# Performance work log

Hardware: AMD Instinct MI355X
Metric: run time of the kernel (lower is better)

Reference implementation:

```python
import jax, jax.numpy as jnp
import numpy as np

N_HEAD = 16

def setup_inputs() -> dict:
    key = jax.random.key(0)
    k1, k2, k3 = jax.random.split(key, 3)
    B, S, D = 2, 2048, 1024
    x = jax.random.normal(k1, (B, S, D), dtype=jnp.float32)
    w_attn = jax.random.normal(k2, (D, 3 * D), dtype=jnp.float32) * 0.02
    b_attn = jnp.zeros((3 * D,), dtype=jnp.float32)
    w_proj = jax.random.normal(k3, (D, D), dtype=jnp.float32) * 0.02
    b_proj = jnp.zeros((D,), dtype=jnp.float32)
    return {"x": x, "w_attn": w_attn, "b_attn": b_attn, "w_proj": w_proj, "b_proj": b_proj}

def reference(x, w_attn, b_attn, w_proj, b_proj):
    B, S, D = x.shape
    hd = D // N_HEAD
    qkv = x @ w_attn + b_attn                      # [B,S,3D]
    q, k, v = jnp.split(qkv, 3, axis=-1)
    def heads(t):  # [B,S,D] -> [B,H,S,hd]
        return t.reshape(B, S, N_HEAD, hd).transpose(0, 2, 1, 3)
    q, k, v = heads(q), heads(k), heads(v)
    # NOTE: original forward applies NO scaling and NO causal mask; dropout=eval (identity)
    scores = jnp.einsum('bhqd,bhkd->bhqk', q, k)   # [B,H,S,S]
    probs = jax.nn.softmax(scores, axis=-1)
    out = jnp.einsum('bhqk,bhkd->bhqd', probs, v)  # [B,H,S,hd]
    out = out.transpose(0, 2, 1, 3).reshape(B, S, D)
    return out @ w_proj + b_proj
```

## Files before the change

### kernel.cpp

```cpp
#include <hip/hip_runtime.h>

typedef _Float16 f16;
typedef _Float16 f16x8 __attribute__((ext_vector_type(8)));
typedef _Float16 f16x4 __attribute__((ext_vector_type(4)));
typedef float    f32x4 __attribute__((ext_vector_type(4)));
typedef unsigned int u32;
typedef unsigned int u32x4 __attribute__((ext_vector_type(4)));

#define LOG2E 1.44269504088896340736f
#define EXPC  (13.0f * 1.44269504088896340736f)

__device__ __forceinline__ void gload_lds16(const void* g, void* l) {
  __builtin_amdgcn_global_load_lds(
      (const __attribute__((address_space(1))) void*)g,
      (__attribute__((address_space(3))) void*)l, 16, 0, 0);
}

__device__ __forceinline__ void block_sync() {
  asm volatile("" ::: "memory");
  __builtin_amdgcn_s_barrier();
  asm volatile("" ::: "memory");
}

__global__ void k_cast_x(const float* __restrict__ in, f16* __restrict__ out) {
  int i = blockIdx.x * blockDim.x + threadIdx.x;
  f32x4 v = ((const f32x4*)in)[i];
  f16x4 o;
  o[0] = (f16)v[0]; o[1] = (f16)v[1]; o[2] = (f16)v[2]; o[3] = (f16)v[3];
  ((f16x4*)out)[i] = o;
}

__global__ void k_transpose_cast(const float* __restrict__ in, f16* __restrict__ out,
                                 int R, int C) {
  __shared__ float tile[32][33];
  int c0 = blockIdx.x * 32, r0 = blockIdx.y * 32;
  int tx = threadIdx.x, ty = threadIdx.y;
#pragma unroll
  for (int i = 0; i < 4; i++)
    tile[ty + i * 8][tx] = in[(size_t)(r0 + ty + i * 8) * C + c0 + tx];
  __syncthreads();
#pragma unroll
  for (int i = 0; i < 4; i++)
    out[(size_t)(c0 + ty + i * 8) * R + r0 + tx] = (f16)tile[tx][ty + i * 8];
}

template <int EPI>
__global__ __launch_bounds__(256)
void k_gemm(const f16* __restrict__ A, const f16* __restrict__ BT,
            const float* __restrict__ bias,
            f16* __restrict__ out_qk, f16* __restrict__ out_vT,
            float* __restrict__ out_f) {
  constexpr int K = 1024;
  __shared__ f16 smem[4][128 * 64];
  const int t = threadIdx.x;
  const int l = t & 63;
  const int w = t >> 6;
  const int wm = (w >> 1) * 64;
  const int wn = (w & 1) * 64;
  const int m0 = blockIdx.x * 128;
  const int n0 = blockIdx.y * 128;
  const int lr = l & 15;
  const int lk = (l >> 4) * 8;

  const f16* Ap = A + (size_t)(m0 + (t >> 3)) * K + ((t & 7) << 3);
  const f16* Bp = BT + (size_t)(n0 + (t >> 3)) * K + ((t & 7) << 3);

#define GSTAGE(buf) do { \
    _Pragma("unroll") \
    for (int i2 = 0; i2 < 4; i2++) \
      gload_lds16(Ap + (size_t)(i2 * 32) * K, &smem[buf][(i2 * 256 + t) * 8]); \
    _Pragma("unroll") \
    for (int i2 = 0; i2 < 4; i2++) \
      gload_lds16(Bp + (size_t)(i2 * 32) * K, &smem[2 + buf][(i2 * 256 + t) * 8]); \
    Ap += 64; Bp += 64; } while (0)

  f32x4 acc[4][4] = {};

#define GCOMPUTE(buf) do { \
    _Pragma("unroll") \
    for (int kk = 0; kk < 64; kk += 32) { \
      f16x8 af[4], bf[4]; \
      _Pragma("unroll") \
      for (int i = 0; i < 4; i++) \
        af[i] = *(const f16x8*)&smem[buf][(wm + i * 16 + lr) * 64 + kk + lk]; \
      _Pragma("unroll") \
      for (int j = 0; j < 4; j++) \
        bf[j] = *(const f16x8*)&smem[2 + buf][(wn + j * 16 + lr) * 64 + kk + lk]; \
      _Pragma("unroll") \
      for (int i = 0; i < 4; i++) \
        _Pragma("unroll") \
        for (int j = 0; j < 4; j++) \
          acc[i][j] = __builtin_amdgcn_mfma_f32_16x16x32_f16(af[i], bf[j], acc[i][j], 0, 0, 0); \
    } } while (0)

  GSTAGE(0);
  asm volatile("s_waitcnt vmcnt(0)" ::: "memory");
  block_sync();

  for (int kt = 0; kt < 16; kt += 2) {
    GSTAGE(1);
    GCOMPUTE(0);
    asm volatile("s_waitcnt vmcnt(0)" ::: "memory");
    block_sync();
    if (kt + 2 < 16) GSTAGE(0);
    GCOMPUTE(1);
    asm volatile("s_waitcnt vmcnt(0)" ::: "memory");
    block_sync();
  }
#undef GSTAGE
#undef GCOMPUTE

  if (EPI == 1) {
#pragma unroll
    for (int i = 0; i < 4; i++) {
      int mbase = m0 + wm + i * 16 + (l >> 4) * 4;
#pragma unroll
      for (int j = 0; j < 4; j++) {
        int n = n0 + wn + j * 16 + lr;
        float bv = bias[n];
#pragma unroll
        for (int r = 0; r < 4; r++)
          out_f[(size_t)(mbase + r) * 1024 + n] = acc[i][j][r] + bv;
      }
    }
  } else if (n0 < 2048) {
#pragma unroll
    for (int i = 0; i < 4; i++) {
      int mbase = m0 + wm + i * 16 + (l >> 4) * 4;
#pragma unroll
      for (int j = 0; j < 4; j++) {
        int n = n0 + wn + j * 16 + lr;
        float bv = bias[n];
        float sc = (n0 + wn + j * 16 < 1024) ? LOG2E : 1.0f;
#pragma unroll
        for (int r = 0; r < 4; r++)
          out_qk[(size_t)(mbase + r) * 2048 + n] = (f16)((acc[i][j][r] + bv) * sc);
      }
    }
  } else {
    f16* scr = &smem[0][0];
#pragma unroll
    for (int i = 0; i < 4; i++) {
      int s0 = wm + i * 16 + (l >> 4) * 4;
#pragma unroll
      for (int j = 0; j < 4; j++) {
        int nl = wn + j * 16 + lr;
        float bv = bias[n0 + nl];
        f16x4 pv;
#pragma unroll
        for (int r = 0; r < 4; r++) pv[r] = (f16)(acc[i][j][r] + bv);
        *(f16x4*)&scr[nl * 128 + (s0 ^ ((nl & 15) << 3))] = pv;
      }
    }
    block_sync();
    const int b = m0 >> 11;
    const int sbase = m0 & 2047;
#pragma unroll
    for (int p = 0; p < 8; p++) {
      int nl = (t >> 4) + p * 16;
      int sc = (t & 15) << 3;
      f16x8 vv = *(const f16x8*)&scr[nl * 128 + (sc ^ ((nl & 15) << 3))];
      int ng = (n0 - 2048) + nl;
      int hg = ng >> 6, d = ng & 63;
      *(f16x8*)&out_vT[(((size_t)(b * 16 + hg) * 64 + d) << 11) + sbase + sc] = vv;
    }
  }
}

__global__ __launch_bounds__(256, 2)
void k_attn(const f16* __restrict__ qk, const f16* __restrict__ vT,
            f16* __restrict__ aout) {
  __shared__ f16 Kl[2][64 * 64];
  __shared__ f16 Vl[2][64 * 64];
  const int t = threadIdx.x;
  const int l = t & 63;
  const int w = t >> 6;
  const int lr = l & 15;
  const int lg = l >> 4;
  const int lk = lg * 8;

  const int o  = (blockIdx.x & 7) * 64 + (blockIdx.x >> 3);
  const int qt = o & 15;
  const int bh = o >> 4;
  const int b  = bh >> 4;
  const int h  = bh & 15;
  const int q0 = qt * 128 + w * 32;

  const f16* qp0 = qk + (size_t)(b * 2048 + q0 + lr) * 2048 + h * 64 + lk;
  const f16* qp1 = qp0 + (size_t)16 * 2048;
  f16x8 qf0 = *(const f16x8*)qp0;
  f16x8 qf1 = *(const f16x8*)(qp0 + 32);
  f16x8 qg0 = *(const f16x8*)qp1;
  f16x8 qg1 = *(const f16x8*)(qp1 + 32);

  const f16* kg = qk + (size_t)(b * 2048) * 2048 + 1024 + h * 64;
  const f16* vg = vT + (size_t)(bh * 64) * 2048;
  const int row8 = t >> 3;
  const int sc0 = (t & 7) ^ (row8 & 7) ^ (row8 >> 3);
  const int off0 = row8 * 2048 + sc0 * 8;
  const int off1 = (row8 + 32) * 2048 + (sc0 ^ 4) * 8;

#define STAGE(B) do { \
    gload_lds16(kg + off0, &Kl[B][t * 8]); \
    gload_lds16(kg + off1, &Kl[B][(256 + t) * 8]); \
    gload_lds16(vg + off0, &Vl[B][t * 8]); \
    gload_lds16(vg + off1, &Vl[B][(256 + t) * 8]); \
    kg += 64 * 2048; vg += 64; } while (0)

  f32x4 oa[4] = {}, ob[4] = {};
  f32x4 ssa = {}, ssb = {};
  const f32x4 initc = {-EXPC, -EXPC, -EXPC, -EXPC};
  f16x8 ones;
#pragma unroll
  for (int j = 0; j < 8; j++) ones[j] = (f16)1.0f;

  STAGE(0);
  asm volatile("s_waitcnt vmcnt(0)" ::: "memory");
  block_sync();

#define TILE_BODY(B) do { \
    f32x4 sa[4], sb[4]; \
    __builtin_amdgcn_s_setprio(1); \
    _Pragma("unroll") \
    for (int c = 0; c < 4; c++) { \
      const int ks = c >> 1, cc = c & 1; \
      const int row = ks * 32 + (lr >> 2) * 8 + (lr & 3) * 2 + cc; \
      const int fr = (row & 7) ^ (row >> 3); \
      f16x8 kf0 = *(const f16x8*)&Kl[B][(row * 8 + (lg ^ fr)) * 8]; \
      f16x8 kf1 = *(const f16x8*)&Kl[B][(row * 8 + ((lg + 4) ^ fr)) * 8]; \
      sa[c] = __builtin_amdgcn_mfma_f32_16x16x32_f16(kf0, qf0, initc, 0, 0, 0); \
      sa[c] = __builtin_amdgcn_mfma_f32_16x16x32_f16(kf1, qf1, sa[c], 0, 0, 0); \
      sb[c] = __builtin_amdgcn_mfma_f32_16x16x32_f16(kf0, qg0, initc, 0, 0, 0); \
      sb[c] = __builtin_amdgcn_mfma_f32_16x16x32_f16(kf1, qg1, sb[c], 0, 0, 0); \
    } \
    __builtin_amdgcn_s_setprio(0); \
    _Pragma("unroll") \
    for (int c = 0; c < 4; c++) \
      _Pragma("unroll") \
      for (int r = 0; r < 4; r++) { \
        sa[c][r] = exp2f(sa[c][r]); \
        sb[c][r] = exp2f(sb[c][r]); \
      } \
    u32 pka[2][4], pkb[2][4]; \
    _Pragma("unroll") \
    for (int ks = 0; ks < 2; ks++) \
      _Pragma("unroll") \
      for (int u = 0; u < 4; u++) { \
        pka[ks][u] = __builtin_bit_cast(u32, \
            __builtin_amdgcn_cvt_pkrtz(sa[2 * ks][u], sa[2 * ks + 1][u])); \
        pkb[ks][u] = __builtin_bit_cast(u32, \
            __builtin_amdgcn_cvt_pkrtz(sb[2 * ks][u], sb[2 * ks + 1][u])); \
      } \
    f16x8 pa0 = __builtin_bit_cast(f16x8, (u32x4){pka[0][0], pka[0][1], pka[0][2], pka[0][3]}); \
    f16x8 pa1 = __builtin_bit_cast(f16x8, (u32x4){pka[1][0], pka[1][1], pka[1][2], pka[1][3]}); \
    f16x8 pb0 = __builtin_bit_cast(f16x8, (u32x4){pkb[0][0], pkb[0][1], pkb[0][2], pkb[0][3]}); \
    f16x8 pb1 = __builtin_bit_cast(f16x8, (u32x4){pkb[1][0], pkb[1][1], pkb[1][2], pkb[1][3]}); \
    __builtin_amdgcn_s_setprio(1); \
    ssa = __builtin_amdgcn_mfma_f32_16x16x32_f16(pa0, ones, ssa, 0, 0, 0); \
    ssa = __builtin_amdgcn_mfma_f32_16x16x32_f16(pa1, ones, ssa, 0, 0, 0); \
    ssb = __builtin_amdgcn_mfma_f32_16x16x32_f16(pb0, ones, ssb, 0, 0, 0); \
    ssb = __builtin_amdgcn_mfma_f32_16x16x32_f16(pb1, ones, ssb, 0, 0, 0); \
    _Pragma("unroll") \
    for (int c4 = 0; c4 < 4; c4++) { \
      const int row = c4 * 16 + lr; \
      const int fr = (row & 7) ^ (row >> 3); \
      f16x8 vf0 = *(const f16x8*)&Vl[B][(row * 8 + (lg ^ fr)) * 8]; \
      f16x8 vf1 = *(const f16x8*)&Vl[B][(row * 8 + ((lg + 4) ^ fr)) * 8]; \
      oa[c4] = __builtin_amdgcn_mfma_f32_16x16x32_f16(pa0, vf0, oa[c4], 0, 0, 0); \
      oa[c4] = __builtin_amdgcn_mfma_f32_16x16x32_f16(pa1, vf1, oa[c4], 0, 0, 0); \
      ob[c4] = __builtin_amdgcn_mfma_f32_16x16x32_f16(pb0, vf0, ob[c4], 0, 0, 0); \
      ob[c4] = __builtin_amdgcn_mfma_f32_16x16x32_f16(pb1, vf1, ob[c4], 0, 0, 0); \
    } \
    __builtin_amdgcn_s_setprio(0); \
    asm volatile("s_waitcnt vmcnt(0)" ::: "memory"); \
    block_sync(); } while (0)

  for (int tt = 0; tt < 32; tt += 2) {
    STAGE(1);
    TILE_BODY(0);
    if (tt + 2 < 32) STAGE(0);
    TILE_BODY(1);
  }
#undef STAGE
#undef TILE_BODY

#pragma unroll
  for (int r = 0; r < 4; r++) {
    float ia = 1.0f / ssa[r];
    float ib = 1.0f / ssb[r];
    size_t rowa = (size_t)(b * 2048 + q0 + lg * 4 + r);
    size_t rowb = rowa + 16;
#pragma unroll
    for (int c4 = 0; c4 < 4; c4++) {
      aout[rowa * 1024 + h * 64 + c4 * 16 + lr] = (f16)(oa[c4][r] * ia);
      aout[rowb * 1024 + h * 64 + c4 * 16 + lr] = (f16)(ob[c4][r] * ib);
    }
  }
}

extern "C" void kernel_launch(void* const* d_in, const int* in_sizes, int n_in,
                              void* d_out, int out_size, void* d_ws, size_t ws_size,
                              hipStream_t stream) {
  const float* x      = (const float*)d_in[0];
  const float* w_attn = (const float*)d_in[1];
  const float* b_attn = (const float*)d_in[2];
  const float* w_proj = (const float*)d_in[3];
  const float* b_proj = (const float*)d_in[4];
  float* out = (float*)d_out;

  char* p = (char*)d_ws;
  f16* xh  = (f16*)p;  p += (size_t)4096 * 1024 * 2;
  f16* waT = (f16*)p;  p += (size_t)3072 * 1024 * 2;
  f16* wpT = (f16*)p;  p += (size_t)1024 * 1024 * 2;
  f16* qkb = (f16*)p;  p += (size_t)4096 * 2048 * 2;
  f16* vTb = (f16*)p;  p += (size_t)32 * 64 * 2048 * 2;
  f16* aob = (f16*)p;  p += (size_t)4096 * 1024 * 2;
  if ((size_t)(p - (char*)d_ws) > ws_size) return;

  k_cast_x<<<4096, 256, 0, stream>>>(x, xh);
  k_transpose_cast<<<dim3(96, 32), dim3(32, 8), 0, stream>>>(w_attn, waT, 1024, 3072);
  k_transpose_cast<<<dim3(32, 32), dim3(32, 8), 0, stream>>>(w_proj, wpT, 1024, 1024);
  k_gemm<0><<<dim3(32, 24), 256, 0, stream>>>(xh, waT, b_attn, qkb, vTb, nullptr);
  k_attn<<<512, 256, 0, stream>>>(qkb, vTb, aob);
  k_gemm<1><<<dim3(32, 8), 256, 0, stream>>>(aob, wpT, b_proj, nullptr, nullptr, out);
}
```

Baseline: 125.7 us.

## Swizzle GEMM LDS tiles and shrink attention blocks to two waves

The GEMM now stores its A/B tiles in LDS with an XOR swizzle on the 16-byte chunk index, and the fragment reads are adjusted to match, to avoid bank conflicts on ds_read. The attention kernel moves from 4-wave blocks over 128 query rows to 2-wave blocks over 64 query rows and launches twice as many blocks. Each thread issues more loads per K/V stage, and the LDS swizzle changes to match. More blocks can raise occupancy and improve load balance, but each K/V tile is now loaded by twice as many blocks, which doubles K/V traffic into LDS.

Result: slower. 135.0 us (+7.4%).

```diff
diff --git a/kernel.cpp b/kernel.cpp
--- a/kernel.cpp
+++ b/kernel.cpp
@@ -60,10 +60,13 @@
   const int m0 = blockIdx.x * 128;
   const int n0 = blockIdx.y * 128;
   const int lr = l & 15;
-  const int lk = (l >> 4) * 8;
-
-  const f16* Ap = A + (size_t)(m0 + (t >> 3)) * K + ((t & 7) << 3);
-  const f16* Bp = BT + (size_t)(n0 + (t >> 3)) * K + ((t & 7) << 3);
+  const int lg = l >> 4;
+  const int fr8 = lr & 7;
+
+  const int row8g = t >> 3;
+  const int scg = (t & 7) ^ (row8g & 7);
+  const f16* Ap = A + (size_t)(m0 + row8g) * K + scg * 8;
+  const f16* Bp = BT + (size_t)(n0 + row8g) * K + scg * 8;
 
 #define GSTAGE(buf) do { \
     _Pragma("unroll") \
@@ -79,13 +82,14 @@
 #define GCOMPUTE(buf) do { \
     _Pragma("unroll") \
     for (int kk = 0; kk < 64; kk += 32) { \
+      const int cbase = (kk >> 3) + lg;   \
       f16x8 af[4], bf[4]; \
       _Pragma("unroll") \
       for (int i = 0; i < 4; i++) \
-        af[i] = *(const f16x8*)&smem[buf][(wm + i * 16 + lr) * 64 + kk + lk]; \
+        af[i] = *(const f16x8*)&smem[buf][((wm + i * 16 + lr) * 8 + (cbase ^ fr8)) * 8]; \
       _Pragma("unroll") \
       for (int j = 0; j < 4; j++) \
-        bf[j] = *(const f16x8*)&smem[2 + buf][(wn + j * 16 + lr) * 64 + kk + lk]; \
+        bf[j] = *(const f16x8*)&smem[2 + buf][((wn + j * 16 + lr) * 8 + (cbase ^ fr8)) * 8]; \
       _Pragma("unroll") \
       for (int i = 0; i < 4; i++) \
         _Pragma("unroll") \
@@ -167,7 +171,7 @@
   }
 }
 
-__global__ __launch_bounds__(256, 2)
+__global__ __launch_bounds__(128, 2)
 void k_attn(const f16* __restrict__ qk, const f16* __restrict__ vT,
             f16* __restrict__ aout) {
   __shared__ f16 Kl[2][64 * 64];
@@ -179,12 +183,12 @@
   const int lg = l >> 4;
   const int lk = lg * 8;
 
-  const int o  = (blockIdx.x & 7) * 64 + (blockIdx.x >> 3);
-  const int qt = o & 15;
-  const int bh = o >> 4;
+  const int o  = (blockIdx.x & 7) * 128 + (blockIdx.x >> 3);
+  const int qt = o & 31;
+  const int bh = o >> 5;
   const int b  = bh >> 4;
   const int h  = bh & 15;
-  const int q0 = qt * 128 + w * 32;
+  const int q0 = qt * 64 + w * 32;
 
   const f16* qp0 = qk + (size_t)(b * 2048 + q0 + lr) * 2048 + h * 64 + lk;
   const f16* qp1 = qp0 + (size_t)16 * 2048;
@@ -195,16 +199,22 @@
 
   const f16* kg = qk + (size_t)(b * 2048) * 2048 + 1024 + h * 64;
   const f16* vg = vT + (size_t)(bh * 64) * 2048;
-  const int row8 = t >> 3;
-  const int sc0 = (t & 7) ^ (row8 & 7) ^ (row8 >> 3);
-  const int off0 = row8 * 2048 + sc0 * 8;
-  const int off1 = (row8 + 32) * 2048 + (sc0 ^ 4) * 8;
+  const int row16 = t >> 3;
+  const int scs = ((t & 7) ^ (row16 & 7)) << 3;
+  const int offA = row16 * 2048 + scs;
+  const int offB = (row16 + 16) * 2048 + scs;
+  const int offC = (row16 + 32) * 2048 + scs;
+  const int offD = (row16 + 48) * 2048 + scs;
 
 #define STAGE(B) do { \
-    gload_lds16(kg + off0, &Kl[B][t * 8]); \
-    gload_lds16(kg + off1, &Kl[B][(256 + t) * 8]); \
-    gload_lds16(vg + off0, &Vl[B][t * 8]); \
-    gload_lds16(vg + off1, &Vl[B][(256 + t) * 8]); \
+    gload_lds16(kg + offA, &Kl[B][t * 8]); \
+    gload_lds16(kg + offB, &Kl[B][(128 + t) * 8]); \
+    gload_lds16(kg + offC, &Kl[B][(256 + t) * 8]); \
+    gload_lds16(kg + offD, &Kl[B][(384 + t) * 8]); \
+    gload_lds16(vg + offA, &Vl[B][t * 8]); \
+    gload_lds16(vg + offB, &Vl[B][(128 + t) * 8]); \
+    gload_lds16(vg + offC, &Vl[B][(256 + t) * 8]); \
+    gload_lds16(vg + offD, &Vl[B][(384 + t) * 8]); \
     kg += 64 * 2048; vg += 64; } while (0)
 
   f32x4 oa[4] = {}, ob[4] = {};
@@ -225,9 +235,9 @@
     for (int c = 0; c < 4; c++) { \
       const int ks = c >> 1, cc = c & 1; \
       const int row = ks * 32 + (lr >> 2) * 8 + (lr & 3) * 2 + cc; \
-      const int fr = (row & 7) ^ (row >> 3); \
-      f16x8 kf0 = *(const f16x8*)&Kl[B][(row * 8 + (lg ^ fr)) * 8]; \
-      f16x8 kf1 = *(const f16x8*)&Kl[B][(row * 8 + ((lg + 4) ^ fr)) * 8]; \
+      const int r7 = row & 7; \
+      f16x8 kf0 = *(const f16x8*)&Kl[B][(row * 8 + (lg ^ r7)) * 8]; \
+      f16x8 kf1 = *(const f16x8*)&Kl[B][(row * 8 + ((lg + 4) ^ r7)) * 8]; \
       sa[c] = __builtin_amdgcn_mfma_f32_16x16x32_f16(kf0, qf0, initc, 0, 0, 0); \
       sa[c] = __builtin_amdgcn_mfma_f32_16x16x32_f16(kf1, qf1, sa[c], 0, 0, 0); \
       sb[c] = __builtin_amdgcn_mfma_f32_16x16x32_f16(kf0, qg0, initc, 0, 0, 0); \
@@ -263,9 +273,9 @@
     _Pragma("unroll") \
     for (int c4 = 0; c4 < 4; c4++) { \
       const int row = c4 * 16 + lr; \
-      const int fr = (row & 7) ^ (row >> 3); \
-      f16x8 vf0 = *(const f16x8*)&Vl[B][(row * 8 + (lg ^ fr)) * 8]; \
-      f16x8 vf1 = *(const f16x8*)&Vl[B][(row * 8 + ((lg + 4) ^ fr)) * 8]; \
+      const int r7 = row & 7; \
+      f16x8 vf0 = *(const f16x8*)&Vl[B][(row * 8 + (lg ^ r7)) * 8]; \
+      f16x8 vf1 = *(const f16x8*)&Vl[B][(row * 8 + ((lg + 4) ^ r7)) * 8]; \
       oa[c4] = __builtin_amdgcn_mfma_f32_16x16x32_f16(pa0, vf0, oa[c4], 0, 0, 0); \
       oa[c4] = __builtin_amdgcn_mfma_f32_16x16x32_f16(pa1, vf1, oa[c4], 0, 0, 0); \
       ob[c4] = __builtin_amdgcn_mfma_f32_16x16x32_f16(pb0, vf0, ob[c4], 0, 0, 0); \
@@ -321,6 +331,6 @@
   k_transpose_cast<<<dim3(96, 32), dim3(32, 8), 0, stream>>>(w_attn, waT, 1024, 3072);
   k_transpose_cast<<<dim3(32, 32), dim3(32, 8), 0, stream>>>(w_proj, wpT, 1024, 1024);
   k_gemm<0><<<dim3(32, 24), 256, 0, stream>>>(xh, waT, b_attn, qkb, vTb, nullptr);
-  k_attn<<<512, 256, 0, stream>>>(qkb, vTb, aob);
+  k_attn<<<1024, 128, 0, stream>>>(qkb, vTb, aob);
   k_gemm<1><<<dim3(32, 8), 256, 0, stream>>>(aob, wpT, b_proj, nullptr, nullptr, out);
 }
```
